# Performance work log

Hardware: AMD Instinct MI355X
Metric: run time of the kernel (lower is better)

Reference implementation:

```python
import jax, jax.numpy as jnp
import numpy as np

N = 20000
E = 320000
IN_DIM = 16
H = 128
HEADS = 4
NEG_SLOPE = 0.2  # GATv2Conv default
EPS_LN = 1e-5


def setup_inputs() -> dict:
    key = jax.random.key(0)
    ks = jax.random.split(key, 16)
    f32 = jnp.float32
    def rn(k, shape, scale):
        return jax.random.normal(k, shape, dtype=f32) * scale
    s_in = 1.0 / np.sqrt(IN_DIM)
    s_h = 1.0 / np.sqrt(H)
    s_4h = 1.0 / np.sqrt(4 * H)
    s_2h = 1.0 / np.sqrt(2 * H)
    inp = {}
    inp["x"] = jax.random.normal(ks[0], (N, IN_DIM), dtype=f32)
    inp["edge_index"] = jax.random.randint(ks[1], (2, E), 0, N)
    inp["edge_attr"] = jax.random.normal(ks[2], (E, 2), dtype=f32)
    inp["emb_w"] = rn(ks[3], (IN_DIM, H), s_in)
    inp["emb_b"] = jnp.zeros((H,), f32)
    # 3 GATv2 layers stacked on leading axis
    inp["lin_l"] = rn(ks[4], (3, H, HEADS * H), s_h)
    inp["lin_r"] = rn(ks[5], (3, H, HEADS * H), s_h)
    inp["lin_edge"] = rn(ks[6], (3, 2, HEADS * H), 1.0 / np.sqrt(2.0))
    inp["att"] = rn(ks[7], (3, HEADS, H), s_h)
    inp["conv_bias01"] = jnp.zeros((2, HEADS * H), f32)  # concat=True layers
    inp["conv_bias2"] = jnp.zeros((H,), f32)             # concat=False layer
    inp["proj_w"] = rn(ks[8], (2, HEADS * H, H), s_4h)
    inp["proj_b"] = jnp.zeros((2, H), f32)
    inp["n1_g"] = jnp.ones((3, H), f32)
    inp["n1_b"] = jnp.zeros((3, H), f32)
    inp["n2_g"] = jnp.ones((3, H), f32)
    inp["n2_b"] = jnp.zeros((3, H), f32)
    inp["ffn_w1"] = rn(ks[9], (3, H, 2 * H), s_h)
    inp["ffn_b1"] = jnp.zeros((3, 2 * H), f32)
    inp["ffn_w2"] = rn(ks[10], (3, 2 * H, H), s_2h)
    inp["ffn_b2"] = jnp.zeros((3, H), f32)
    return inp


def layer_norm(x, g, b):
    mu = jnp.mean(x, axis=-1, keepdims=True)
    var = jnp.mean((x - mu) ** 2, axis=-1, keepdims=True)
    return (x - mu) * jax.lax.rsqrt(var + EPS_LN) * g + b


def gatv2(h, src, dst, eattr, Wl, Wr, We, att, bias, concat, n):
    # h: [n, H]; per-edge gather -> GATv2 attention -> segment softmax -> scatter-add
    xl = (h @ Wl).reshape(n, HEADS, H)   # source transform
    xr = (h @ Wr).reshape(n, HEADS, H)   # target transform
    ee = (eattr @ We).reshape(-1, HEADS, H)
    e = jax.nn.leaky_relu(xl[src] + xr[dst] + ee, NEG_SLOPE)  # [E', HEADS, H]
    score = jnp.einsum('ehc,hc->eh', e, att)                  # [E', HEADS]
    smax = jax.ops.segment_max(score, dst, num_segments=n)
    p = jnp.exp(score - smax[dst])
    denom = jax.ops.segment_sum(p, dst, num_segments=n)
    alpha = p / (denom[dst] + 1e-16)
    out = jax.ops.segment_sum(xl[src] * alpha[..., None], dst, num_segments=n)
    if concat:
        return out.reshape(n, HEADS * H) + bias
    return jnp.mean(out, axis=1) + bias


def reference(x, edge_index, edge_attr, emb_w, emb_b, lin_l, lin_r, lin_edge, att,
              conv_bias01, conv_bias2, proj_w, proj_b, n1_g, n1_b, n2_g, n2_b,
              ffn_w1, ffn_b1, ffn_w2, ffn_b2):
    n = x.shape[0]
    e = edge_attr.shape[0]
    # PyG add_self_loops with fill_value='mean': self-loop attr = mean of incoming edge attrs
    ones = jnp.ones((e,), x.dtype)
    deg = jax.ops.segment_sum(ones, edge_index[1], num_segments=n)
    loop_attr = jax.ops.segment_sum(edge_attr, edge_index[1], num_segments=n) / jnp.maximum(deg, 1.0)[:, None]
    ar = jnp.arange(n)
    src = jnp.concatenate([edge_index[0], ar])
    dst = jnp.concatenate([edge_index[1], ar])
    ea = jnp.concatenate([edge_attr, loop_attr], axis=0)

    h = x @ emb_w + emb_b
    for i in range(3):
        concat = i < 2
        bias = conv_bias01[i] if concat else conv_bias2
        h_in = h
        h = gatv2(h, src, dst, ea, lin_l[i], lin_r[i], lin_edge[i], att[i], bias, concat, n)
        if concat:
            h = h @ proj_w[i] + proj_b[i]
        h = layer_norm(h + h_in, n1_g[i], n1_b[i])
        h2 = h
        h = jax.nn.gelu(h @ ffn_w1[i] + ffn_b1[i], approximate=False) @ ffn_w2[i] + ffn_b2[i]
        h = layer_norm(h + h2, n2_g[i], n2_b[i])
    return h
```

## Files before the change

### kernel.cpp

```cpp
#include <hip/hip_runtime.h>
#include <math.h>

#define IN_DIM 16
#define HDIM   128
#define HEADS  4
#define HH     512
#define FFH    256
#define NEG_SLOPE 0.2f

typedef _Float16 half8 __attribute__((ext_vector_type(8)));
typedef _Float16 h8 __attribute__((ext_vector_type(8)));
typedef _Float16 h4 __attribute__((ext_vector_type(4)));
typedef _Float16 h2 __attribute__((ext_vector_type(2)));
typedef float f32x4 __attribute__((ext_vector_type(4)));

struct __align__(8) Edge { int src; _Float16 ea0, ea1; };

static __device__ inline float hsum8(h8 v) {
    h4 a = __builtin_shufflevector(v, v, 0, 1, 2, 3) +
           __builtin_shufflevector(v, v, 4, 5, 6, 7);
    h2 b = __builtin_shufflevector(a, a, 0, 1) +
           __builtin_shufflevector(a, a, 2, 3);
    return (float)b[0] + (float)b[1];
}

__global__ void xpad_kernel(const float* __restrict__ x, _Float16* __restrict__ xh, int n) {
    int idx = blockIdx.x * 256 + threadIdx.x;
    if (idx >= n * 64) return;
    int r = idx >> 6, k = idx & 63;
    xh[idx] = (k < IN_DIM) ? (_Float16)x[r * IN_DIM + k] : (_Float16)0.0f;
}

struct WDesc { const float* src; _Float16* dst; int Ksrc; int lgKd; int lgN; };
struct WDescs { WDesc d[15]; };
__global__ void wconv_kernel(WDescs ds) {
    WDesc w = ds.d[blockIdx.y];
    int Kd = 1 << w.lgKd;
    int total = 1 << (w.lgKd + w.lgN);
    for (int idx = blockIdx.x * 256 + threadIdx.x; idx < total; idx += gridDim.x * 256) {
        int n2 = idx >> w.lgKd, k = idx & (Kd - 1);
        w.dst[idx] = (k < w.Ksrc) ? (_Float16)w.src[(k << w.lgN) + n2] : (_Float16)0.0f;
    }
}

__global__ void deg_kernel(const int* __restrict__ ei, const float* __restrict__ eattr,
                           float* deg, float* asum, int E) {
    int e = blockIdx.x * blockDim.x + threadIdx.x;
    if (e >= E) return;
    int d = ei[E + e];
    atomicAdd(&deg[d], 1.0f);
    atomicAdd(&asum[2 * d], eattr[2 * e]);
    atomicAdd(&asum[2 * d + 1], eattr[2 * e + 1]);
}

__global__ void scan_kernel(const float* __restrict__ deg, int* row_ptr, int* cur, int n) {
    __shared__ int sums[1024];
    int tid = threadIdx.x;
    int per = (n + 1023) / 1024;
    int s0 = tid * per;
    int s1 = s0 + per; if (s1 > n) s1 = n;
    int s = 0;
    for (int i = s0; i < s1; i++) s += (int)deg[i] + 1;
    int mysum = s;
    sums[tid] = s;
    __syncthreads();
    for (int dd = 1; dd < 1024; dd <<= 1) {
        int t = (tid >= dd) ? sums[tid - dd] : 0;
        __syncthreads();
        sums[tid] += t;
        __syncthreads();
    }
    int run = sums[tid] - mysum;
    for (int i = s0; i < s1; i++) {
        row_ptr[i] = run; cur[i] = run;
        run += (int)deg[i] + 1;
    }
    if (tid == 1023) row_ptr[n] = sums[1023];
}

__global__ void scatter_kernel(const int* __restrict__ ei, const float* __restrict__ eattr,
                               const float* __restrict__ deg, const float* __restrict__ asum,
                               int* cur, Edge* csr, int E, int n) {
    int i = blockIdx.x * blockDim.x + threadIdx.x;
    if (i >= E + n) return;
    Edge ed;
    int pos;
    if (i < E) {
        int d = ei[E + i];
        pos = atomicAdd(&cur[d], 1);
        ed.src = ei[i];
        ed.ea0 = (_Float16)eattr[2 * i];
        ed.ea1 = (_Float16)eattr[2 * i + 1];
    } else {
        int nd = i - E;
        float dv = fmaxf(deg[nd], 1.0f);
        pos = atomicAdd(&cur[nd], 1);
        ed.src = nd;
        ed.ea0 = (_Float16)(asum[2 * nd] / dv);
        ed.ea1 = (_Float16)(asum[2 * nd + 1] / dv);
    }
    csr[pos] = ed;
}

template <int KT, int OUTMODE>
__global__ __launch_bounds__(256) void gemm_bstat(const _Float16* __restrict__ A, int lda,
                                                  const _Float16* __restrict__ BT,
                                                  const float* __restrict__ bias,
                                                  float* __restrict__ C32,
                                                  _Float16* __restrict__ C16,
                                                  int M, int Nstride, int numMT) {
    const int PAD = 8, KC = KT / 32;
    __shared__ _Float16 Bs[128][KT + PAD];
    int tid = threadIdx.x;
    int wave = tid >> 6, lane = tid & 63;
    int quad = lane >> 4, l16 = lane & 15;
    int wrow = (wave >> 1) * 32, wcol = (wave & 1) * 64;
    int n0 = blockIdx.x * 128;

#pragma unroll
    for (int t = 0; t < KT / 16; t++) {
        int idx = tid + t * 256;
        int r = idx / (KT / 8), kb = (idx % (KT / 8)) * 8;
        *(half8*)&Bs[r][kb] = *(const half8*)(BT + (size_t)(n0 + r) * KT + kb);
    }
    __syncthreads();

    half8 bfrag[4][KC];
#pragma unroll
    for (int j = 0; j < 4; j++)
#pragma unroll
        for (int kc = 0; kc < KC; kc++)
            bfrag[j][kc] = *(const half8*)&Bs[wcol + j * 16 + l16][kc * 32 + quad * 8];

    float biasj[4];
#pragma unroll
    for (int j = 0; j < 4; j++)
        biasj[j] = bias ? bias[n0 + wcol + j * 16 + l16] : 0.0f;

    for (int mt = blockIdx.y; mt < numMT; mt += gridDim.y) {
        int rbase = mt * 64 + wrow;
        half8 af[2][KC];
#pragma unroll
        for (int i = 0; i < 2; i++) {
            int row = rbase + i * 16 + l16;
#pragma unroll
            for (int kc = 0; kc < KC; kc++)
                af[i][kc] = (row < M) ? *(const half8*)(A + (size_t)row * lda + kc * 32 + quad * 8)
                                      : (half8)(_Float16)0.0f;
        }
        f32x4 acc[2][4] = {};
#pragma unroll
        for (int kc = 0; kc < KC; kc++)
#pragma unroll
            for (int i = 0; i < 2; i++)
#pragma unroll
                for (int j = 0; j < 4; j++)
                    acc[i][j] = __builtin_amdgcn_mfma_f32_16x16x32_f16(af[i][kc], bfrag[j][kc], acc[i][j], 0, 0, 0);
#pragma unroll
        for (int i = 0; i < 2; i++) {
#pragma unroll
            for (int r = 0; r < 4; r++) {
                int row = rbase + i * 16 + quad * 4 + r;
                if (row >= M) continue;
#pragma unroll
                for (int j = 0; j < 4; j++) {
                    int col = n0 + wcol + j * 16 + l16;
                    float v = acc[i][j][r] + biasj[j];
                    if (OUTMODE == 2)
                        C32[(size_t)row * Nstride + col] = v;
                    C16[(size_t)row * Nstride + col] = (_Float16)v;
                }
            }
        }
    }
}

__global__ __launch_bounds__(256) void gemm_ln(const _Float16* __restrict__ A, int lda,
                                               const _Float16* __restrict__ BT,
                                               const float* __restrict__ bias,
                                               const float* __restrict__ R,
                                               const float* __restrict__ g,
                                               const float* __restrict__ b,
                                               float* __restrict__ C32,
                                               _Float16* __restrict__ C16,
                                               int M, int K) {
    const int BK = 64, PAD = 8;
    __shared__ _Float16 As[64][BK + PAD];
    __shared__ _Float16 Bs[128][BK + PAD];
    int tid = threadIdx.x;
    int wave = tid >> 6, lane = tid & 63;
    int quad = lane >> 4, l16 = lane & 15;
    int mBase = blockIdx.x * 64;

    f32x4 acc[8] = {};

    for (int k0 = 0; k0 < K; k0 += BK) {
#pragma unroll
        for (int t = 0; t < 2; t++) {
            int idx = tid + t * 256;
            int r = idx >> 3, kb = (idx & 7) * 8;
            half8 hv = {};
            int grow = mBase + r;
            if (grow < M) hv = *(const half8*)(A + (size_t)grow * lda + k0 + kb);
            *(half8*)&As[r][kb] = hv;
        }
#pragma unroll
        for (int t = 0; t < 4; t++) {
            int idx = tid + t * 256;
            int r = idx >> 3, kb = (idx & 7) * 8;
            *(half8*)&Bs[r][kb] = *(const half8*)(BT + (size_t)r * K + k0 + kb);
        }
        __syncthreads();
#pragma unroll
        for (int kc = 0; kc < 2; kc++) {
            half8 a = *(const half8*)&As[wave * 16 + l16][kc * 32 + quad * 8];
#pragma unroll
            for (int j = 0; j < 8; j++) {
                half8 bb = *(const half8*)&Bs[j * 16 + l16][kc * 32 + quad * 8];
                acc[j] = __builtin_amdgcn_mfma_f32_16x16x32_f16(a, bb, acc[j], 0, 0, 0);
            }
        }
        __syncthreads();
    }

    float gj[8], bj[8], biasj[8];
#pragma unroll
    for (int j = 0; j < 8; j++) {
        int col = j * 16 + l16;
        biasj[j] = bias[col];
        gj[j] = g[col];
        bj[j] = b[col];
    }
    int row0 = mBase + wave * 16 + quad * 4;
    float sum[4] = {}, sq[4] = {};
#pragma unroll
    for (int r = 0; r < 4; r++) {
        int row = row0 + r;
        bool ok = row < M;
        size_t base = (size_t)row * HDIM;
#pragma unroll
        for (int j = 0; j < 8; j++) {
            float v = acc[j][r] + biasj[j] + (ok ? R[base + j * 16 + l16] : 0.0f);
            acc[j][r] = v;
            sum[r] += v;
            sq[r] += v * v;
        }
    }
#pragma unroll
    for (int r = 0; r < 4; r++) {
#pragma unroll
        for (int off = 1; off < 16; off <<= 1) {
            sum[r] += __shfl_xor(sum[r], off);
            sq[r] += __shfl_xor(sq[r], off);
        }
    }
#pragma unroll
    for (int r = 0; r < 4; r++) {
        int row = row0 + r;
        if (row >= M) continue;
        size_t base = (size_t)row * HDIM;
        float mu = sum[r] * (1.0f / HDIM);
        float var = sq[r] * (1.0f / HDIM) - mu * mu;
        float invstd = rsqrtf(var + 1e-5f);
#pragma unroll
        for (int j = 0; j < 8; j++) {
            float o = (acc[j][r] - mu) * invstd * gj[j] + bj[j];
            C32[base + j * 16 + l16] = o;
            if (C16) C16[base + j * 16 + l16] = (_Float16)o;
        }
    }
}

__global__ __launch_bounds__(256) void ffn_fused(const _Float16* __restrict__ A,
                                                 const _Float16* __restrict__ W1T,
                                                 const float* __restrict__ b1,
                                                 const _Float16* __restrict__ W2T,
                                                 const float* __restrict__ b2,
                                                 const float* __restrict__ R,
                                                 const float* __restrict__ g,
                                                 const float* __restrict__ b,
                                                 float* __restrict__ C32,
                                                 _Float16* __restrict__ C16,
                                                 int M) {
    __shared__ _Float16 Ws[128][128 + 8];
    __shared__ _Float16 Mid[64][256 + 8];
    int tid = threadIdx.x;
    int wave = tid >> 6, lane = tid & 63;
    int quad = lane >> 4, l16 = lane & 15;
    int mBase = blockIdx.x * 64;

    half8 afrag[4];
    {
        int row = mBase + wave * 16 + l16;
#pragma unroll
        for (int kc = 0; kc < 4; kc++) {
            if (row < M)
                afrag[kc] = *(const half8*)(A + (size_t)row * HDIM + kc * 32 + quad * 8);
            else
                afrag[kc] = (half8)(_Float16)0.0f;
        }
    }

#pragma unroll
    for (int h = 0; h < 2; h++) {
        if (h) __syncthreads();
#pragma unroll
        for (int t = 0; t < 8; t++) {
            int idx = tid + t * 256;
            int r = idx >> 4, kb = (idx & 15) * 8;
            *(half8*)&Ws[r][kb] = *(const half8*)(W1T + (size_t)(h * 128 + r) * HDIM + kb);
        }
        __syncthreads();
        f32x4 acc[8] = {};
#pragma unroll
        for (int kc = 0; kc < 4; kc++) {
#pragma unroll
            for (int j = 0; j < 8; j++) {
                half8 bb = *(const half8*)&Ws[j * 16 + l16][kc * 32 + quad * 8];
                acc[j] = __builtin_amdgcn_mfma_f32_16x16x32_f16(afrag[kc], bb, acc[j], 0, 0, 0);
            }
        }
#pragma unroll
        for (int j = 0; j < 8; j++) {
            float bj1 = b1[h * 128 + j * 16 + l16];
#pragma unroll
            for (int r = 0; r < 4; r++) {
                float v = acc[j][r] + bj1;
                v = 0.5f * v * (1.0f + erff(v * 0.70710678118654752f));
                Mid[wave * 16 + quad * 4 + r][h * 128 + j * 16 + l16] = (_Float16)v;
            }
        }
    }
    __syncthreads();

    f32x4 acc2[8] = {};
#pragma unroll
    for (int kc2 = 0; kc2 < 2; kc2++) {
        if (kc2) __syncthreads();
#pragma unroll
        for (int t = 0; t < 8; t++) {
            int idx = tid + t * 256;
            int r = idx >> 4, kb = (idx & 15) * 8;
            *(half8*)&Ws[r][kb] = *(const half8*)(W2T + (size_t)r * FFH + kc2 * 128 + kb);
        }
        __syncthreads();
#pragma unroll
        for (int kc = 0; kc < 4; kc++) {
            half8 am = *(const half8*)&Mid[wave * 16 + l16][kc2 * 128 + kc * 32 + quad * 8];
#pragma unroll
            for (int j = 0; j < 8; j++) {
                half8 bb = *(const half8*)&Ws[j * 16 + l16][kc * 32 + quad * 8];
                acc2[j] = __builtin_amdgcn_mfma_f32_16x16x32_f16(am, bb, acc2[j], 0, 0, 0);
            }
        }
    }

    float gj[8], bj[8], b2j[8];
#pragma unroll
    for (int j = 0; j < 8; j++) {
        int col = j * 16 + l16;
        b2j[j] = b2[col];
        gj[j] = g[col];
        bj[j] = b[col];
    }
    int row0 = mBase + wave * 16 + quad * 4;
    float sum[4] = {}, sq[4] = {};
#pragma unroll
    for (int r = 0; r < 4; r++) {
        int row = row0 + r;
        bool ok = row < M;
        size_t base = (size_t)row * HDIM;
#pragma unroll
        for (int j = 0; j < 8; j++) {
            float v = acc2[j][r] + b2j[j] + (ok ? R[base + j * 16 + l16] : 0.0f);
            acc2[j][r] = v;
            sum[r] += v;
            sq[r] += v * v;
        }
    }
#pragma unroll
    for (int r = 0; r < 4; r++) {
#pragma unroll
        for (int off = 1; off < 16; off <<= 1) {
            sum[r] += __shfl_xor(sum[r], off);
            sq[r] += __shfl_xor(sq[r], off);
        }
    }
#pragma unroll
    for (int r = 0; r < 4; r++) {
        int row = row0 + r;
        if (row >= M) continue;
        size_t base = (size_t)row * HDIM;
        float mu = sum[r] * (1.0f / HDIM);
        float var = sq[r] * (1.0f / HDIM) - mu * mu;
        float invstd = rsqrtf(var + 1e-5f);
#pragma unroll
        for (int j = 0; j < 8; j++) {
            float o = (acc2[j][r] - mu) * invstd * gj[j] + bj[j];
            C32[base + j * 16 + l16] = o;
            if (C16) C16[base + j * 16 + l16] = (_Float16)o;
        }
    }
}

__global__ __launch_bounds__(256) void gat_edge_kernel(
    const _Float16* __restrict__ XLR,
    const int* __restrict__ row_ptr, const Edge* __restrict__ csr,
    const float* __restrict__ We,
    const float* __restrict__ attW,
    const float* __restrict__ cbias,
    _Float16* __restrict__ OUT16, float* __restrict__ OUT32,
    const float* __restrict__ R, const float* __restrict__ lng,
    const float* __restrict__ lnb, _Float16* __restrict__ OUT16h,
    int n, int concat) {
    int tid = threadIdx.x;
    int wave = tid >> 6, lane = tid & 63;
    int node = blockIdx.x * 4 + wave;
    if (node >= n) return;
    int c0 = lane * 8;

    h8 xr8 = *(const h8*)(XLR + (size_t)node * 1024 + 512 + c0);
    h8 w08, w18, att8;
#pragma unroll
    for (int k = 0; k < 8; k++) {
        w08[k] = (_Float16)We[c0 + k];
        w18[k] = (_Float16)We[HH + c0 + k];
        att8[k] = (_Float16)attW[c0 + k];
    }
    const _Float16 slope = (_Float16)NEG_SLOPE;

    h8 acc2 = (h8)(_Float16)0.0f;
    float m = -INFINITY, l = 0.0f;
    int beg = row_ptr[node], end = row_ptr[node + 1];
    int j = beg;
    for (; j + 1 < end; j += 2) {
        Edge e0 = csr[j], e1 = csr[j + 1];
        h8 x0 = *(const h8*)(XLR + (size_t)e0.src * 1024 + c0);
        h8 x1 = *(const h8*)(XLR + (size_t)e1.src * 1024 + c0);
        h8 v0 = x0 + (xr8 + w08 * e0.ea0 + w18 * e0.ea1);
        h8 v1 = x1 + (xr8 + w08 * e1.ea0 + w18 * e1.ea1);
        v0 = __builtin_elementwise_max(v0, v0 * slope);
        v1 = __builtin_elementwise_max(v1, v1 * slope);
        float p0 = hsum8(v0 * att8);
        float p1 = hsum8(v1 * att8);
        p0 += __shfl_xor(p0, 1); p1 += __shfl_xor(p1, 1);
        p0 += __shfl_xor(p0, 2); p1 += __shfl_xor(p1, 2);
        p0 += __shfl_xor(p0, 4); p1 += __shfl_xor(p1, 4);
        p0 += __shfl_xor(p0, 8); p1 += __shfl_xor(p1, 8);
        float mnew = fmaxf(m, fmaxf(p0, p1));
        float sc = __expf(m - mnew);
        float e0f = __expf(p0 - mnew);
        float e1f = __expf(p1 - mnew);
        l = l * sc + e0f + e1f;
        acc2 = acc2 * (_Float16)sc + x0 * (_Float16)e0f + x1 * (_Float16)e1f;
        m = mnew;
    }
    if (j < end) {
        Edge e0 = csr[j];
        h8 x0 = *(const h8*)(XLR + (size_t)e0.src * 1024 + c0);
        h8 v0 = x0 + (xr8 + w08 * e0.ea0 + w18 * e0.ea1);
        v0 = __builtin_elementwise_max(v0, v0 * slope);
        float p0 = hsum8(v0 * att8);
        p0 += __shfl_xor(p0, 1);
        p0 += __shfl_xor(p0, 2);
        p0 += __shfl_xor(p0, 4);
        p0 += __shfl_xor(p0, 8);
        float mnew = fmaxf(m, p0);
        float sc = __expf(m - mnew);
        float e0f = __expf(p0 - mnew);
        l = l * sc + e0f;
        acc2 = acc2 * (_Float16)sc + x0 * (_Float16)e0f;
        m = mnew;
    }
    float invf = 1.0f / (l + 1e-16f);
    if (concat) {
        h8 o = acc2 * (_Float16)invf;
#pragma unroll
        for (int k = 0; k < 8; k++) o[k] = o[k] + (_Float16)cbias[c0 + k];
        *(h8*)(OUT16 + (size_t)node * 1024 + c0) = o;
    } else {
        float o8[8];
#pragma unroll
        for (int k = 0; k < 8; k++) {
            float a = (float)acc2[k] * invf;
            a += __shfl_xor(a, 16);
            a += __shfl_xor(a, 32);
            o8[k] = a;
        }
        float v8[8];
        float sum = 0.0f, sq = 0.0f;
        if (lane < 16) {
#pragma unroll
            for (int k = 0; k < 8; k++) {
                float v = o8[k] * 0.25f + cbias[c0 + k] + R[(size_t)node * HDIM + c0 + k];
                v8[k] = v;
                sum += v;
                sq += v * v;
            }
        }
#pragma unroll
        for (int off = 1; off < 16; off <<= 1) {
            sum += __shfl_xor(sum, off);
            sq += __shfl_xor(sq, off);
        }
        if (lane < 16) {
            float mu = sum * (1.0f / HDIM);
            float var = sq * (1.0f / HDIM) - mu * mu;
            float invstd = rsqrtf(var + 1e-5f);
#pragma unroll
            for (int k = 0; k < 8; k++) {
                float o = (v8[k] - mu) * invstd * lng[c0 + k] + lnb[c0 + k];
                OUT32[(size_t)node * HDIM + c0 + k] = o;
                OUT16h[(size_t)node * HDIM + c0 + k] = (_Float16)o;
            }
        }
    }
}

extern "C" void kernel_launch(void* const* d_in, const int* in_sizes, int n_in,
                              void* d_out, int out_size, void* d_ws, size_t ws_size,
                              hipStream_t stream) {
    const float* x        = (const float*)d_in[0];
    const int*   ei       = (const int*)d_in[1];
    const float* eattr    = (const float*)d_in[2];
    const float* emb_w    = (const float*)d_in[3];
    const float* emb_b    = (const float*)d_in[4];
    const float* lin_l    = (const float*)d_in[5];
    const float* lin_r    = (const float*)d_in[6];
    const float* lin_edge = (const float*)d_in[7];
    const float* attw     = (const float*)d_in[8];
    const float* cb01     = (const float*)d_in[9];
    const float* cb2      = (const float*)d_in[10];
    const float* proj_w   = (const float*)d_in[11];
    const float* proj_b   = (const float*)d_in[12];
    const float* n1g      = (const float*)d_in[13];
    const float* n1b      = (const float*)d_in[14];
    const float* n2g      = (const float*)d_in[15];
    const float* n2b      = (const float*)d_in[16];
    const float* fw1      = (const float*)d_in[17];
    const float* fb1      = (const float*)d_in[18];
    const float* fw2      = (const float*)d_in[19];
    const float* fb2      = (const float*)d_in[20];
    float* out = (float*)d_out;

    const int n = in_sizes[0] / IN_DIM;
    const int E = in_sizes[2] / 2;
    const int EP = E + n;
    const int numMT = (n + 63) / 64;

    size_t off = 0;
    auto alloc = [&](size_t bytes) {
        void* p = (char*)d_ws + off;
        off += (bytes + 255) & ~(size_t)255;
        return p;
    };
    float* deg     = (float*)alloc((size_t)n * 4);
    float* asum    = (float*)alloc((size_t)2 * n * 4);
    int*   row_ptr = (int*)alloc((size_t)(n + 1) * 4);
    int*   cur     = (int*)alloc((size_t)n * 4);
    Edge*  csr     = (Edge*)alloc((size_t)EP * 8);
    float* H0      = (float*)alloc((size_t)n * HDIM * 4);
    float* H1      = (float*)alloc((size_t)n * HDIM * 4);
    _Float16* H0h  = (_Float16*)alloc((size_t)n * HDIM * 2);
    _Float16* H1h  = (_Float16*)alloc((size_t)n * HDIM * 2);
    _Float16* XLR  = (_Float16*)alloc((size_t)n * 1024 * 2);
    _Float16* xh   = (_Float16*)alloc((size_t)n * 64 * 2);
    _Float16* wt_emb  = (_Float16*)alloc((size_t)HDIM * 64 * 2);
    _Float16* wt_llr  = (_Float16*)alloc((size_t)3 * 1024 * HDIM * 2);
    _Float16* wt_proj = (_Float16*)alloc((size_t)2 * HDIM * HH * 2);
    _Float16* wt_f1   = (_Float16*)alloc((size_t)3 * FFH * HDIM * 2);
    _Float16* wt_f2   = (_Float16*)alloc((size_t)3 * HDIM * FFH * 2);
    (void)ws_size;

    xpad_kernel<<<(n * 64 + 255) / 256, 256, 0, stream>>>(x, xh, n);
    WDescs ds;
    int di = 0;
    ds.d[di++] = {emb_w, wt_emb, IN_DIM, 6, 7};
    for (int i = 0; i < 3; i++) {
        ds.d[di++] = {lin_l + (size_t)i * HDIM * HH, wt_llr + (size_t)i * 1024 * HDIM, HDIM, 7, 9};
        ds.d[di++] = {lin_r + (size_t)i * HDIM * HH, wt_llr + (size_t)i * 1024 * HDIM + (size_t)512 * HDIM, HDIM, 7, 9};
    }
    for (int i = 0; i < 2; i++)
        ds.d[di++] = {proj_w + (size_t)i * HH * HDIM, wt_proj + (size_t)i * HDIM * HH, HH, 9, 7};
    for (int i = 0; i < 3; i++)
        ds.d[di++] = {fw1 + (size_t)i * HDIM * FFH, wt_f1 + (size_t)i * FFH * HDIM, HDIM, 7, 8};
    for (int i = 0; i < 3; i++)
        ds.d[di++] = {fw2 + (size_t)i * FFH * HDIM, wt_f2 + (size_t)i * HDIM * FFH, FFH, 8, 7};
    wconv_kernel<<<dim3(32, 15), 256, 0, stream>>>(ds);

    (void)hipMemsetAsync(deg, 0, (size_t)n * 4, stream);
    (void)hipMemsetAsync(asum, 0, (size_t)2 * n * 4, stream);
    deg_kernel<<<(E + 255) / 256, 256, 0, stream>>>(ei, eattr, deg, asum, E);
    scan_kernel<<<1, 1024, 0, stream>>>(deg, row_ptr, cur, n);
    scatter_kernel<<<(EP + 255) / 256, 256, 0, stream>>>(ei, eattr, deg, asum, cur, csr, E, n);

    gemm_bstat<64, 2><<<dim3(1, numMT), 256, 0, stream>>>(
        xh, 64, wt_emb, emb_b, H0, H0h, n, HDIM, numMT);

    for (int i = 0; i < 3; i++) {
        int concat = (i < 2);
        gemm_bstat<128, 1><<<dim3(8, 80), 256, 0, stream>>>(
            H0h, HDIM, wt_llr + (size_t)i * 1024 * HDIM, nullptr,
            nullptr, XLR, n, 1024, numMT);
        gat_edge_kernel<<<(n + 3) / 4, 256, 0, stream>>>(
            XLR, row_ptr, csr,
            lin_edge + (size_t)i * 2 * HH, attw + (size_t)i * HH,
            concat ? (cb01 + (size_t)i * HH) : cb2,
            XLR + 512, H1,
            H0, n1g + (size_t)i * HDIM, n1b + (size_t)i * HDIM, H1h,
            n, concat);
        if (concat) {
            gemm_ln<<<(n + 63) / 64, 256, 0, stream>>>(
                XLR + 512, 1024, wt_proj + (size_t)i * HDIM * HH,
                proj_b + (size_t)i * HDIM, H0,
                n1g + (size_t)i * HDIM, n1b + (size_t)i * HDIM,
                H1, H1h, n, HH);
        }
        float* lnout = (i == 2) ? out : H0;
        _Float16* lnout16 = (i == 2) ? nullptr : H0h;
        ffn_fused<<<(n + 63) / 64, 256, 0, stream>>>(
            H1h, wt_f1 + (size_t)i * FFH * HDIM, fb1 + (size_t)i * FFH,
            wt_f2 + (size_t)i * HDIM * FFH, fb2 + (size_t)i * HDIM, H1,
            n2g + (size_t)i * HDIM, n2b + (size_t)i * HDIM,
            lnout, lnout16, n);
    }
}
```

Measured before the change: 568.7 us.

## Split each node's edge list across two waves and merge softmax partials in LDS

The GAT edge kernel now gives each destination node two waves, each running the online-softmax gather over half of the incoming edges. The second wave writes its running max, sum and accumulator to shared memory, and the first wave combines the two partial states after a block barrier. The goal is to shorten each wave's serial, latency-bound gather chain and double the number of waves in flight. In exchange, setup loads are duplicated, a __syncthreads and LDS traffic are added, and half of the waves sit idle during the epilogue.

```diff
diff --git a/kernel.cpp b/kernel.cpp
--- a/kernel.cpp
+++ b/kernel.cpp
@@ -413,13 +413,17 @@
     const float* __restrict__ R, const float* __restrict__ lng,
     const float* __restrict__ lnb, _Float16* __restrict__ OUT16h,
     int n, int concat) {
+    __shared__ float sM[2][64], sL[2][64];
+    __shared__ h8 sAcc[2][64];
     int tid = threadIdx.x;
     int wave = tid >> 6, lane = tid & 63;
-    int node = blockIdx.x * 4 + wave;
-    if (node >= n) return;
+    int nodeIdx = wave >> 1;
+    int half = wave & 1;
+    int node = blockIdx.x * 2 + nodeIdx;
+    bool active = node < n;
     int c0 = lane * 8;
 
-    h8 xr8 = *(const h8*)(XLR + (size_t)node * 1024 + 512 + c0);
+    h8 xr8 = (h8)(_Float16)0.0f;
     h8 w08, w18, att8;
 #pragma unroll
     for (int k = 0; k < 8; k++) {
@@ -431,47 +435,73 @@
 
     h8 acc2 = (h8)(_Float16)0.0f;
     float m = -INFINITY, l = 0.0f;
-    int beg = row_ptr[node], end = row_ptr[node + 1];
-    int j = beg;
-    for (; j + 1 < end; j += 2) {
-        Edge e0 = csr[j], e1 = csr[j + 1];
-        h8 x0 = *(const h8*)(XLR + (size_t)e0.src * 1024 + c0);
-        h8 x1 = *(const h8*)(XLR + (size_t)e1.src * 1024 + c0);
-        h8 v0 = x0 + (xr8 + w08 * e0.ea0 + w18 * e0.ea1);
-        h8 v1 = x1 + (xr8 + w08 * e1.ea0 + w18 * e1.ea1);
-        v0 = __builtin_elementwise_max(v0, v0 * slope);
-        v1 = __builtin_elementwise_max(v1, v1 * slope);
-        float p0 = hsum8(v0 * att8);
-        float p1 = hsum8(v1 * att8);
-        p0 += __shfl_xor(p0, 1); p1 += __shfl_xor(p1, 1);
-        p0 += __shfl_xor(p0, 2); p1 += __shfl_xor(p1, 2);
-        p0 += __shfl_xor(p0, 4); p1 += __shfl_xor(p1, 4);
-        p0 += __shfl_xor(p0, 8); p1 += __shfl_xor(p1, 8);
-        float mnew = fmaxf(m, fmaxf(p0, p1));
-        float sc = __expf(m - mnew);
-        float e0f = __expf(p0 - mnew);
-        float e1f = __expf(p1 - mnew);
-        l = l * sc + e0f + e1f;
-        acc2 = acc2 * (_Float16)sc + x0 * (_Float16)e0f + x1 * (_Float16)e1f;
-        m = mnew;
-    }
-    if (j < end) {
-        Edge e0 = csr[j];
-        h8 x0 = *(const h8*)(XLR + (size_t)e0.src * 1024 + c0);
-        h8 v0 = x0 + (xr8 + w08 * e0.ea0 + w18 * e0.ea1);
-        v0 = __builtin_elementwise_max(v0, v0 * slope);
-        float p0 = hsum8(v0 * att8);
-        p0 += __shfl_xor(p0, 1);
-        p0 += __shfl_xor(p0, 2);
-        p0 += __shfl_xor(p0, 4);
-        p0 += __shfl_xor(p0, 8);
-        float mnew = fmaxf(m, p0);
-        float sc = __expf(m - mnew);
-        float e0f = __expf(p0 - mnew);
-        l = l * sc + e0f;
-        acc2 = acc2 * (_Float16)sc + x0 * (_Float16)e0f;
-        m = mnew;
-    }
+
+    if (active) {
+        xr8 = *(const h8*)(XLR + (size_t)node * 1024 + 512 + c0);
+        int beg = row_ptr[node], end = row_ptr[node + 1];
+        int mid = beg + ((end - beg + 1) >> 1);
+        int b0 = half ? mid : beg;
+        int e0 = half ? end : mid;
+        int j = b0;
+        for (; j + 1 < e0; j += 2) {
+            Edge eg0 = csr[j], eg1 = csr[j + 1];
+            h8 x0 = *(const h8*)(XLR + (size_t)eg0.src * 1024 + c0);
+            h8 x1 = *(const h8*)(XLR + (size_t)eg1.src * 1024 + c0);
+            h8 v0 = x0 + (xr8 + w08 * eg0.ea0 + w18 * eg0.ea1);
+            h8 v1 = x1 + (xr8 + w08 * eg1.ea0 + w18 * eg1.ea1);
+            v0 = __builtin_elementwise_max(v0, v0 * slope);
+            v1 = __builtin_elementwise_max(v1, v1 * slope);
+            float p0 = hsum8(v0 * att8);
+            float p1 = hsum8(v1 * att8);
+            p0 += __shfl_xor(p0, 1); p1 += __shfl_xor(p1, 1);
+            p0 += __shfl_xor(p0, 2); p1 += __shfl_xor(p1, 2);
+            p0 += __shfl_xor(p0, 4); p1 += __shfl_xor(p1, 4);
+            p0 += __shfl_xor(p0, 8); p1 += __shfl_xor(p1, 8);
+            float mnew = fmaxf(m, fmaxf(p0, p1));
+            float sc = __expf(m - mnew);
+            float e0f = __expf(p0 - mnew);
+            float e1f = __expf(p1 - mnew);
+            l = l * sc + e0f + e1f;
+            acc2 = acc2 * (_Float16)sc + x0 * (_Float16)e0f + x1 * (_Float16)e1f;
+            m = mnew;
+        }
+        if (j < e0) {
+            Edge eg0 = csr[j];
+            h8 x0 = *(const h8*)(XLR + (size_t)eg0.src * 1024 + c0);
+            h8 v0 = x0 + (xr8 + w08 * eg0.ea0 + w18 * eg0.ea1);
+            v0 = __builtin_elementwise_max(v0, v0 * slope);
+            float p0 = hsum8(v0 * att8);
+            p0 += __shfl_xor(p0, 1);
+            p0 += __shfl_xor(p0, 2);
+            p0 += __shfl_xor(p0, 4);
+            p0 += __shfl_xor(p0, 8);
+            float mnew = fmaxf(m, p0);
+            float sc = __expf(m - mnew);
+            float e0f = __expf(p0 - mnew);
+            l = l * sc + e0f;
+            acc2 = acc2 * (_Float16)sc + x0 * (_Float16)e0f;
+            m = mnew;
+        }
+    }
+
+    if (half == 1) {
+        sM[nodeIdx][lane] = m;
+        sL[nodeIdx][lane] = l;
+        sAcc[nodeIdx][lane] = acc2;
+    }
+    __syncthreads();
+    if (half != 0 || !active) return;
+    {
+        float mB = sM[nodeIdx][lane];
+        float lB = sL[nodeIdx][lane];
+        h8 accB = sAcc[nodeIdx][lane];
+        float mS = fmaxf(m, mB);
+        float sA = __expf(m - mS);
+        float sB = __expf(mB - mS);
+        l = l * sA + lB * sB;
+        acc2 = acc2 * (_Float16)sA + accB * (_Float16)sB;
+    }
+
     float invf = 1.0f / (l + 1e-16f);
     if (concat) {
         h8 o = acc2 * (_Float16)invf;
@@ -602,7 +632,7 @@
         gemm_bstat<128, 1><<<dim3(8, 80), 256, 0, stream>>>(
             H0h, HDIM, wt_llr + (size_t)i * 1024 * HDIM, nullptr,
             nullptr, XLR, n, 1024, numMT);
-        gat_edge_kernel<<<(n + 3) / 4, 256, 0, stream>>>(
+        gat_edge_kernel<<<(n + 1) / 2, 256, 0, stream>>>(
             XLR, row_ptr, csr,
             lin_edge + (size_t)i * 2 * HH, attw + (size_t)i * HH,
             concat ? (cb01 + (size_t)i * HH) : cb2,
```

After: 564.9 us. No clear change (-0.7%).
